# Kernel optimization log

Measured on AMD Instinct MI355X. Metric: run time of the kernel, lower is better.

## Reference

```python
import jax, jax.numpy as jnp
import numpy as np

HEADS, DIM_HEAD = 8, 64
EPS = 1e-5  # torch InstanceNorm1d default


def instance_norm(t):
    # torch InstanceNorm1d(dim_head) applied to (b*h, n, d) normalizes over the
    # last dim d for each (b, h, n); affine=False, biased variance.
    mu = jnp.mean(t, axis=-1, keepdims=True)
    var = jnp.mean((t - mu) ** 2, axis=-1, keepdims=True)
    return (t - mu) * jax.lax.rsqrt(var + EPS)


def setup_inputs() -> dict:
    key = jax.random.key(0)
    k1, k2, k3, k4 = jax.random.split(key, 4)
    B, N, D = 8, 8192, 256
    inner = HEADS * DIM_HEAD  # 512
    x = jax.random.normal(k1, (B, N, D), jnp.float32)
    w_qkv = jax.random.normal(k2, (3 * inner, D), jnp.float32) / np.sqrt(D).astype(np.float32)
    w_out = jax.random.normal(k3, (D, inner), jnp.float32) / np.sqrt(inner).astype(np.float32)
    b_out = 0.01 * jax.random.normal(k4, (D,), jnp.float32)
    return {"x": x, "w_qkv": w_qkv, "w_out": w_out, "b_out": b_out}


def reference(x, w_qkv, w_out, b_out):
    B, N, _ = x.shape
    H, Dh = HEADS, DIM_HEAD
    # fused qkv projection: [B,N,3*H*Dh]
    qkv = jnp.einsum('bnd,ed->bne', x, w_qkv)
    q, k, v = jnp.split(qkv, 3, axis=-1)

    def to_heads(t):
        return t.reshape(B, N, H, Dh).transpose(0, 2, 1, 3)  # b h n d

    q, k, v = to_heads(q), to_heads(k), to_heads(v)
    # galerkin: instance-norm K and V
    k = instance_norm(k)
    v = instance_norm(v)
    # linear (non-softmax) attention: (K^T V) then Q @ (K^T V), scaled by 1/N
    dots = jnp.einsum('bhnd,bhne->bhde', k, v)            # [B,H,Dh,Dh]
    out = jnp.einsum('bhnd,bhde->bhne', q, dots) / N      # [B,H,N,Dh]
    out = out.transpose(0, 2, 1, 3).reshape(B, N, H * Dh)
    return jnp.einsum('bne,de->bnd', out, w_out) + b_out
```

## Files before the change

### kernel.cpp

```cpp
#include <hip/hip_runtime.h>
#include <hip/hip_bf16.h>
#include <stdint.h>

typedef __attribute__((ext_vector_type(8))) __bf16 bf16x8;
typedef __attribute__((ext_vector_type(8))) unsigned short ushort8_t;
typedef __attribute__((ext_vector_type(4))) unsigned short ushort4_t;
typedef __attribute__((ext_vector_type(4))) float f32x4;

#define MFMA16(a, b, c) __builtin_amdgcn_mfma_f32_16x16x32_bf16((a), (b), (c), 0, 0, 0)

static __device__ __forceinline__ unsigned short f2bf(float f) {
  union { float f; unsigned u; } v; v.f = f;
  unsigned r = v.u + 0x7fffu + ((v.u >> 16) & 1u);
  return (unsigned short)(r >> 16);
}
static __device__ __forceinline__ float bf2f(unsigned short u) {
  union { unsigned u; float f; } v; v.u = ((unsigned)u) << 16; return v.f;
}

static __device__ __forceinline__ void gld_lds16(const void* g, void* l) {
  __builtin_amdgcn_global_load_lds((const __attribute__((address_space(1))) void*)g,
                                   (__attribute__((address_space(3))) void*)l, 16, 0, 0);
}

__global__ __launch_bounds__(256) void k_convx(const float* __restrict__ x,
                                               unsigned short* __restrict__ xb) {
  size_t i = ((size_t)blockIdx.x * 256 + threadIdx.x) * 4;
  float4 v = *(const float4*)(x + i);
  ushort4_t o = { f2bf(v.x), f2bf(v.y), f2bf(v.z), f2bf(v.w) };
  *(ushort4_t*)(xb + i) = o;
}

__global__ void k_convw(const float* __restrict__ w, unsigned short* __restrict__ wb) {
  int i = (blockIdx.x * 256 + threadIdx.x) * 4;
  float4 v = *(const float4*)(w + i);
  ushort4_t o = { f2bf(v.x), f2bf(v.y), f2bf(v.z), f2bf(v.w) };
  *(ushort4_t*)(wb + i) = o;
}

__global__ __launch_bounds__(512) void k_gemm1(const unsigned short* __restrict__ xb,
                                               const unsigned short* __restrict__ wqb,
                                               unsigned short* __restrict__ qkv) {
  __shared__ unsigned short As[2][16384];
  __shared__ unsigned short Bs[2][16384];
  const int t = threadIdx.x;
  const int w = t >> 6, lane = t & 63, lr = lane & 15, lg = lane >> 4;
  const int wr = w >> 2, wc = w & 3;

  const int id = blockIdx.x;
  const int nid = (id & 7) * 192 + (id >> 3);
  const int nt = nid % 6, mt = nid / 6;
  const long m0 = (long)mt * 256;
  const int e0 = nt * 256;

  const int srl = lane >> 3, sc = lane & 7;

#pragma unroll
  for (int i = 0; i < 2; ++i) {
    const int r = (w * 2 + i) * 8 + srl;
    const int cs = (sc ^ (r & 7)) << 3;
    gld_lds16(xb + (size_t)(m0 + r) * 256 + cs,          &As[0][(w * 2 + i) * 512]);
    gld_lds16(xb + (size_t)(m0 + 128 + r) * 256 + cs,    &As[0][8192 + (w * 2 + i) * 512]);
    gld_lds16(wqb + (size_t)(e0 + r) * 256 + cs,         &Bs[0][(w * 2 + i) * 512]);
    gld_lds16(wqb + (size_t)(e0 + 128 + r) * 256 + cs,   &Bs[0][8192 + (w * 2 + i) * 512]);
  }
  __syncthreads();

  f32x4 acc[8][4];
#pragma unroll
  for (int i = 0; i < 8; ++i)
#pragma unroll
    for (int j = 0; j < 4; ++j) acc[i][j] = f32x4{0.f, 0.f, 0.f, 0.f};

  bf16x8 a[4][2], b[2][2][2];

  for (int kt = 0; kt < 4; ++kt) {
    const int cur = kt & 1, nxt = cur ^ 1;
    const int kn0 = (kt + 1) * 64;
    const bool st = kt < 3;

#pragma unroll
    for (int mb = 0; mb < 4; ++mb) {
      const int R = wr * 128 + mb * 16 + lr;
#pragma unroll
      for (int kh = 0; kh < 2; ++kh)
        a[mb][kh] = *(const bf16x8*)&As[cur][R * 64 + ((((kh << 2) + lg) ^ (R & 7)) << 3)];
    }
#pragma unroll
    for (int nb = 0; nb < 2; ++nb) {
      const int E = wc * 64 + nb * 16 + lr;
#pragma unroll
      for (int kh = 0; kh < 2; ++kh)
        b[0][nb][kh] = *(const bf16x8*)&Bs[cur][E * 64 + ((((kh << 2) + lg) ^ (E & 7)) << 3)];
    }
    if (st) {
#pragma unroll
      for (int i = 0; i < 2; ++i) {
        const int r = (w * 2 + i) * 8 + srl;
        gld_lds16(xb + (size_t)(m0 + r) * 256 + kn0 + ((sc ^ (r & 7)) << 3),
                  &As[nxt][(w * 2 + i) * 512]);
      }
    }
    __builtin_amdgcn_s_barrier();
    __builtin_amdgcn_s_setprio(1);
#pragma unroll
    for (int mb = 0; mb < 4; ++mb)
#pragma unroll
      for (int nb = 0; nb < 2; ++nb)
#pragma unroll
        for (int kh = 0; kh < 2; ++kh)
          acc[mb][nb] = MFMA16(a[mb][kh], b[0][nb][kh], acc[mb][nb]);
    __builtin_amdgcn_s_setprio(0);
    __builtin_amdgcn_s_barrier();

#pragma unroll
    for (int nb = 0; nb < 2; ++nb) {
      const int E = wc * 64 + 32 + nb * 16 + lr;
#pragma unroll
      for (int kh = 0; kh < 2; ++kh)
        b[1][nb][kh] = *(const bf16x8*)&Bs[cur][E * 64 + ((((kh << 2) + lg) ^ (E & 7)) << 3)];
    }
    if (st) {
#pragma unroll
      for (int i = 0; i < 2; ++i) {
        const int r = (w * 2 + i) * 8 + srl;
        gld_lds16(xb + (size_t)(m0 + 128 + r) * 256 + kn0 + ((sc ^ (r & 7)) << 3),
                  &As[nxt][8192 + (w * 2 + i) * 512]);
      }
    }
    __builtin_amdgcn_s_barrier();
    __builtin_amdgcn_s_setprio(1);
#pragma unroll
    for (int mb = 0; mb < 4; ++mb)
#pragma unroll
      for (int nb = 0; nb < 2; ++nb)
#pragma unroll
        for (int kh = 0; kh < 2; ++kh)
          acc[mb][2 + nb] = MFMA16(a[mb][kh], b[1][nb][kh], acc[mb][2 + nb]);
    __builtin_amdgcn_s_setprio(0);
    __builtin_amdgcn_s_barrier();

#pragma unroll
    for (int mb = 0; mb < 4; ++mb) {
      const int R = wr * 128 + 64 + mb * 16 + lr;
#pragma unroll
      for (int kh = 0; kh < 2; ++kh)
        a[mb][kh] = *(const bf16x8*)&As[cur][R * 64 + ((((kh << 2) + lg) ^ (R & 7)) << 3)];
    }
    if (st) {
#pragma unroll
      for (int i = 0; i < 2; ++i) {
        const int r = (w * 2 + i) * 8 + srl;
        gld_lds16(wqb + (size_t)(e0 + r) * 256 + kn0 + ((sc ^ (r & 7)) << 3),
                  &Bs[nxt][(w * 2 + i) * 512]);
      }
    }
    __builtin_amdgcn_s_barrier();
    __builtin_amdgcn_s_setprio(1);
#pragma unroll
    for (int mb = 0; mb < 4; ++mb)
#pragma unroll
      for (int nb = 0; nb < 2; ++nb)
#pragma unroll
        for (int kh = 0; kh < 2; ++kh)
          acc[4 + mb][nb] = MFMA16(a[mb][kh], b[0][nb][kh], acc[4 + mb][nb]);
    __builtin_amdgcn_s_setprio(0);
    __builtin_amdgcn_s_barrier();

    if (st) {
#pragma unroll
      for (int i = 0; i < 2; ++i) {
        const int r = (w * 2 + i) * 8 + srl;
        gld_lds16(wqb + (size_t)(e0 + 128 + r) * 256 + kn0 + ((sc ^ (r & 7)) << 3),
                  &Bs[nxt][8192 + (w * 2 + i) * 512]);
      }
    }
    __builtin_amdgcn_s_barrier();
    __builtin_amdgcn_s_setprio(1);
#pragma unroll
    for (int mb = 0; mb < 4; ++mb)
#pragma unroll
      for (int nb = 0; nb < 2; ++nb)
#pragma unroll
        for (int kh = 0; kh < 2; ++kh)
          acc[4 + mb][2 + nb] = MFMA16(a[mb][kh], b[1][nb][kh], acc[4 + mb][2 + nb]);
    __builtin_amdgcn_s_setprio(0);
    __syncthreads();
  }

#pragma unroll
  for (int i = 0; i < 8; ++i) {
    const long row0 = m0 + wr * 128 + (i >> 2) * 64 + (i & 3) * 16 + lg * 4;
#pragma unroll
    for (int j = 0; j < 4; ++j) {
      const int col = e0 + wc * 64 + (j >> 1) * 32 + (j & 1) * 16 + lr;
#pragma unroll
      for (int rg = 0; rg < 4; ++rg)
        qkv[(size_t)(row0 + rg) * 1536 + col] = f2bf(acc[i][j][rg]);
    }
  }
}

__global__ __launch_bounds__(256) void k_dots(const unsigned short* __restrict__ qkv,
                                              float* __restrict__ partials) {
  __shared__ unsigned short ktl[2][64 * 72];
  __shared__ unsigned short vtl[2][64 * 72];
  const int bh = blockIdx.x, ch = blockIdx.y;
  const int b = bh >> 3, h = bh & 7;
  const int t = threadIdx.x;
  const int w = t >> 6, lane = t & 63, lr = lane & 15, lg = lane >> 4;
  const unsigned short* kbase = qkv + ((size_t)b * 8192) * 1536 + 512 + h * 64;
  const int r = t >> 2, q4 = t & 3;
  const int n00 = ch * 1024;
  f32x4 acc[4];
#pragma unroll
  for (int eb = 0; eb < 4; ++eb) acc[eb] = f32x4{0.f, 0.f, 0.f, 0.f};

  ushort8_t rA[4], rB[4];
  {
    const unsigned short* krow = kbase + (size_t)(n00 + r) * 1536 + q4 * 16;
    rA[0] = *(const ushort8_t*)krow;
    rA[1] = *(const ushort8_t*)(krow + 8);
    rA[2] = *(const ushort8_t*)(krow + 512);
    rA[3] = *(const ushort8_t*)(krow + 520);
  }

#define DOTS_BODY(RC, RN, NT)                                                     \
  {                                                                               \
    float kf[16], vf[16];                                                         \
    _Pragma("unroll") for (int i = 0; i < 8; ++i) {                               \
      kf[i] = bf2f(RC[0][i]); kf[i + 8] = bf2f(RC[1][i]);                         \
      vf[i] = bf2f(RC[2][i]); vf[i + 8] = bf2f(RC[3][i]);                         \
    }                                                                             \
    float ksum = 0, ksq = 0, vsum = 0, vsq = 0;                                   \
    _Pragma("unroll") for (int i = 0; i < 16; ++i) {                              \
      ksum += kf[i]; ksq += kf[i] * kf[i];                                        \
      vsum += vf[i]; vsq += vf[i] * vf[i];                                        \
    }                                                                             \
    ksum += __shfl_xor(ksum, 1); ksq += __shfl_xor(ksq, 1);                       \
    vsum += __shfl_xor(vsum, 1); vsq += __shfl_xor(vsq, 1);                       \
    ksum += __shfl_xor(ksum, 2); ksq += __shfl_xor(ksq, 2);                       \
    vsum += __shfl_xor(vsum, 2); vsq += __shfl_xor(vsq, 2);                       \
    const float kmean = ksum * (1.f / 64.f);                                      \
    const float krs = rsqrtf(ksq * (1.f / 64.f) - kmean * kmean + 1e-5f);         \
    const float vmean = vsum * (1.f / 64.f);                                      \
    const float vrs = rsqrtf(vsq * (1.f / 64.f) - vmean * vmean + 1e-5f);         \
    const int cu = (NT) & 1;                                                      \
    _Pragma("unroll") for (int i = 0; i < 16; ++i) {                              \
      int d = q4 * 16 + i;                                                        \
      ktl[cu][d * 72 + r] = f2bf((kf[i] - kmean) * krs);                          \
      vtl[cu][d * 72 + r] = f2bf((vf[i] - vmean) * vrs);                          \
    }                                                                             \
    if ((NT) + 1 < 16) {                                                          \
      const unsigned short* krow2 =                                               \
          kbase + (size_t)(n00 + ((NT) + 1) * 64 + r) * 1536 + q4 * 16;           \
      RN[0] = *(const ushort8_t*)krow2;                                           \
      RN[1] = *(const ushort8_t*)(krow2 + 8);                                     \
      RN[2] = *(const ushort8_t*)(krow2 + 512);                                   \
      RN[3] = *(const ushort8_t*)(krow2 + 520);                                   \
    }                                                                             \
    __syncthreads();                                                              \
    _Pragma("unroll") for (int ns = 0; ns < 64; ns += 32) {                       \
      bf16x8 af = *(const bf16x8*)&ktl[cu][(16 * w + lr) * 72 + ns + lg * 8];     \
      _Pragma("unroll") for (int eb = 0; eb < 4; ++eb) {                          \
        bf16x8 bv = *(const bf16x8*)&vtl[cu][(16 * eb + lr) * 72 + ns + lg * 8];  \
        acc[eb] = MFMA16(af, bv, acc[eb]);                                        \
      }                                                                           \
    }                                                                             \
  }

  for (int nt = 0; nt < 16; nt += 2) {
    DOTS_BODY(rA, rB, nt);
    DOTS_BODY(rB, rA, nt + 1);
  }
#undef DOTS_BODY

  float* pb = partials + ((size_t)ch * 64 + bh) * 4096;
#pragma unroll
  for (int eb = 0; eb < 4; ++eb)
#pragma unroll
    for (int rg = 0; rg < 4; ++rg) {
      int d = 16 * w + lg * 4 + rg;
      int e = 16 * eb + lr;
      pb[d * 64 + e] = acc[eb][rg];
    }
}

__global__ __launch_bounds__(256) void k_mmat(const float* __restrict__ partials,
                                              const float* __restrict__ wout,
                                              unsigned short* __restrict__ mswz) {
  __shared__ float dl[4096];
  const int bh = blockIdx.x, b = bh >> 3, h = bh & 7;
  const int t = threadIdx.x;
#pragma unroll
  for (int i = 0; i < 4; ++i) {
    int off = t * 16 + i * 4;
    f32x4 s = {0.f, 0.f, 0.f, 0.f};
    for (int c = 0; c < 8; ++c) {
      f32x4 p = *(const f32x4*)(partials + ((size_t)c * 64 + bh) * 4096 + off);
      s += p;
    }
    *(f32x4*)&dl[off] = s;
  }
  __syncthreads();
  float wrow[64];
#pragma unroll
  for (int e = 0; e < 64; e += 4) {
    f32x4 v = *(const f32x4*)(wout + (size_t)t * 512 + h * 64 + e);
    wrow[e] = v[0]; wrow[e + 1] = v[1]; wrow[e + 2] = v[2]; wrow[e + 3] = v[3];
  }
  const float scale = 1.0f / 8192.0f;
  for (int d = 0; d < 64; ++d) {
    float s = 0.f;
#pragma unroll
    for (int e = 0; e < 64; ++e) s += dl[d * 64 + e] * wrow[e];
    s *= scale;
    int kk = h * 64 + d;
    int kblk = kk >> 5, j = kk & 7;
    int lane8 = ((kk >> 3) & 3) * 16 + (t & 15);
    int nblk = t >> 4;
    mswz[(size_t)b * 131072 + ((size_t)(kblk * 16 + nblk) * 64 + lane8) * 8 + j] = f2bf(s);
  }
}

__global__ __launch_bounds__(512) void k_gemm2(const unsigned short* __restrict__ qkv,
                                               const unsigned short* __restrict__ mswz,
                                               const float* __restrict__ bout,
                                               float* __restrict__ out) {
  __shared__ unsigned short As[2][128 * 64];
  const int b = blockIdx.x >> 6, mt = blockIdx.x & 63;
  const long m0 = (long)mt * 128;
  const int t = threadIdx.x, w = t >> 6, lane = t & 63, lr = lane & 15, lg = lane >> 4;
  const int wr = w >> 2, wc = w & 3;
  const unsigned short* qb = qkv + ((size_t)b * 8192 + m0) * 1536;
  const unsigned short* Mb = mswz + (size_t)b * 131072;
  const int srl = lane >> 3, sc = lane & 7;

#pragma unroll
  for (int i = 0; i < 2; ++i) {
    const int row = (i * 8 + w) * 8 + srl;
    gld_lds16(qb + (size_t)row * 1536 + ((sc ^ (row & 7)) << 3),
              &As[0][(i * 8 + w) * 512]);
  }
  __syncthreads();

  f32x4 acc[4][4];
#pragma unroll
  for (int mb = 0; mb < 4; ++mb)
#pragma unroll
    for (int nb = 0; nb < 4; ++nb) acc[mb][nb] = f32x4{0.f, 0.f, 0.f, 0.f};

  for (int ks = 0; ks < 8; ++ks) {
    const int cur = ks & 1, nxt = cur ^ 1;
    if (ks < 7) {
      const int k0 = (ks + 1) * 64;
#pragma unroll
      for (int i = 0; i < 2; ++i) {
        const int row = (i * 8 + w) * 8 + srl;
        gld_lds16(qb + (size_t)row * 1536 + k0 + ((sc ^ (row & 7)) << 3),
                  &As[nxt][(i * 8 + w) * 512]);
      }
    }
    bf16x8 a[4][2], bfr[2][4];
#pragma unroll
    for (int mb = 0; mb < 4; ++mb) {
      const int R = wr * 64 + mb * 16 + lr;
#pragma unroll
      for (int kh = 0; kh < 2; ++kh)
        a[mb][kh] = *(const bf16x8*)&As[cur][R * 64 + ((((kh << 2) + lg) ^ (R & 7)) << 3)];
    }
#pragma unroll
    for (int kh = 0; kh < 2; ++kh)
#pragma unroll
      for (int nb = 0; nb < 4; ++nb)
        bfr[kh][nb] = *(const bf16x8*)(Mb + ((((size_t)ks * 2 + kh) * 16 + wc * 4 + nb) * 64 + lane) * 8);
#pragma unroll
    for (int mb = 0; mb < 4; ++mb)
#pragma unroll
      for (int nb = 0; nb < 4; ++nb)
#pragma unroll
        for (int kh = 0; kh < 2; ++kh)
          acc[mb][nb] = MFMA16(a[mb][kh], bfr[kh][nb], acc[mb][nb]);
    __syncthreads();
  }

  float bo[4];
#pragma unroll
  for (int nb = 0; nb < 4; ++nb) bo[nb] = bout[wc * 64 + nb * 16 + lr];
  float* ob = out + ((size_t)b * 8192 + m0) * 256;
#pragma unroll
  for (int mb = 0; mb < 4; ++mb)
#pragma unroll
    for (int nb = 0; nb < 4; ++nb)
#pragma unroll
      for (int rg = 0; rg < 4; ++rg) {
        int row = wr * 64 + mb * 16 + lg * 4 + rg;
        int c = wc * 64 + nb * 16 + lr;
        ob[(size_t)row * 256 + c] = acc[mb][nb][rg] + bo[nb];
      }
}

extern "C" void kernel_launch(void* const* d_in, const int* in_sizes, int n_in,
                              void* d_out, int out_size, void* d_ws, size_t ws_size,
                              hipStream_t stream) {
  const float* x    = (const float*)d_in[0];
  const float* wqkv = (const float*)d_in[1];
  const float* wout = (const float*)d_in[2];
  const float* bout = (const float*)d_in[3];
  float* out = (float*)d_out;

  char* ws = (char*)d_ws;
  unsigned short* qkvb = (unsigned short*)ws;
  size_t off = (size_t)65536 * 1536 * 2;
  unsigned short* wqb = (unsigned short*)(ws + off);
  off += (size_t)1536 * 256 * 2;
  float* partials = (float*)(ws + off);
  off += (size_t)8 * 64 * 4096 * 4;
  unsigned short* mswz = (unsigned short*)(ws + off);
  off += (size_t)8 * 131072 * 2;
  unsigned short* xb = (unsigned short*)(ws + off);
  off += (size_t)65536 * 256 * 2;

  k_convx<<<16384, 256, 0, stream>>>(x, xb);
  k_convw<<<384, 256, 0, stream>>>(wqkv, wqb);
  k_gemm1<<<1536, 512, 0, stream>>>(xb, wqb, qkvb);
  dim3 gd(64, 8);
  k_dots<<<gd, 256, 0, stream>>>(qkvb, partials);
  k_mmat<<<64, 256, 0, stream>>>(partials, wout, mswz);
  k_gemm2<<<512, 512, 0, stream>>>(qkvb, mswz, bout, out);
}
```

Before: 195.2 us.

## Fold Q projection into per-batch output matrix, skip computing Q

Instead of materialising Q through the first GEMM, the Q weight slice is folded algebraically into a per-batch 256x256 matrix P = W_out * (dots^T W_q / N) built by the new k_mmat/k_pmat kernels. The first GEMM now only produces K and V (1024 columns), and the final GEMM reads bf16 x with K=256 instead of Q with K=512. This removes a third of the large projection GEMM and its write, and halves the output GEMM's reduction and reads. In exchange it adds two small kernels, an extra bf16 rounding of the fused matrix, and a W_out conversion.

```diff
diff --git a/kernel.cpp b/kernel.cpp
--- a/kernel.cpp
+++ b/kernel.cpp
@@ -38,9 +38,16 @@
   *(ushort4_t*)(wb + i) = o;
 }
 
+__global__ void k_convo(const float* __restrict__ w, unsigned short* __restrict__ wb) {
+  int i = (blockIdx.x * 256 + threadIdx.x) * 4;
+  float4 v = *(const float4*)(w + i);
+  ushort4_t o = { f2bf(v.x), f2bf(v.y), f2bf(v.z), f2bf(v.w) };
+  *(ushort4_t*)(wb + i) = o;
+}
+
 __global__ __launch_bounds__(512) void k_gemm1(const unsigned short* __restrict__ xb,
                                                const unsigned short* __restrict__ wqb,
-                                               unsigned short* __restrict__ qkv) {
+                                               unsigned short* __restrict__ kvb) {
   __shared__ unsigned short As[2][16384];
   __shared__ unsigned short Bs[2][16384];
   const int t = threadIdx.x;
@@ -48,10 +55,10 @@
   const int wr = w >> 2, wc = w & 3;
 
   const int id = blockIdx.x;
-  const int nid = (id & 7) * 192 + (id >> 3);
-  const int nt = nid % 6, mt = nid / 6;
+  const int nid = (id & 7) * 128 + (id >> 3);
+  const int nt = nid & 3, mt = nid >> 2;
   const long m0 = (long)mt * 256;
-  const int e0 = nt * 256;
+  const int e0 = 512 + nt * 256;
 
   const int srl = lane >> 3, sc = lane & 7;
 
@@ -193,15 +200,15 @@
     const long row0 = m0 + wr * 128 + (i >> 2) * 64 + (i & 3) * 16 + lg * 4;
 #pragma unroll
     for (int j = 0; j < 4; ++j) {
-      const int col = e0 + wc * 64 + (j >> 1) * 32 + (j & 1) * 16 + lr;
+      const int col = nt * 256 + wc * 64 + (j >> 1) * 32 + (j & 1) * 16 + lr;
 #pragma unroll
       for (int rg = 0; rg < 4; ++rg)
-        qkv[(size_t)(row0 + rg) * 1536 + col] = f2bf(acc[i][j][rg]);
-    }
-  }
-}
-
-__global__ __launch_bounds__(256) void k_dots(const unsigned short* __restrict__ qkv,
+        kvb[(size_t)(row0 + rg) * 1024 + col] = f2bf(acc[i][j][rg]);
+    }
+  }
+}
+
+__global__ __launch_bounds__(256) void k_dots(const unsigned short* __restrict__ kvb,
                                               float* __restrict__ partials) {
   __shared__ unsigned short ktl[2][64 * 72];
   __shared__ unsigned short vtl[2][64 * 72];
@@ -209,7 +216,7 @@
   const int b = bh >> 3, h = bh & 7;
   const int t = threadIdx.x;
   const int w = t >> 6, lane = t & 63, lr = lane & 15, lg = lane >> 4;
-  const unsigned short* kbase = qkv + ((size_t)b * 8192) * 1536 + 512 + h * 64;
+  const unsigned short* kbase = kvb + ((size_t)b * 8192) * 1024 + h * 64;
   const int r = t >> 2, q4 = t & 3;
   const int n00 = ch * 1024;
   f32x4 acc[4];
@@ -218,7 +225,7 @@
 
   ushort8_t rA[4], rB[4];
   {
-    const unsigned short* krow = kbase + (size_t)(n00 + r) * 1536 + q4 * 16;
+    const unsigned short* krow = kbase + (size_t)(n00 + r) * 1024 + q4 * 16;
     rA[0] = *(const ushort8_t*)krow;
     rA[1] = *(const ushort8_t*)(krow + 8);
     rA[2] = *(const ushort8_t*)(krow + 512);
@@ -253,7 +260,7 @@
     }                                                                             \
     if ((NT) + 1 < 16) {                                                          \
       const unsigned short* krow2 =                                               \
-          kbase + (size_t)(n00 + ((NT) + 1) * 64 + r) * 1536 + q4 * 16;           \
+          kbase + (size_t)(n00 + ((NT) + 1) * 64 + r) * 1024 + q4 * 16;           \
       RN[0] = *(const ushort8_t*)krow2;                                           \
       RN[1] = *(const ushort8_t*)(krow2 + 8);                                     \
       RN[2] = *(const ushort8_t*)(krow2 + 512);                                   \
@@ -287,9 +294,10 @@
 }
 
 __global__ __launch_bounds__(256) void k_mmat(const float* __restrict__ partials,
-                                              const float* __restrict__ wout,
-                                              unsigned short* __restrict__ mswz) {
+                                              const float* __restrict__ wqkv,
+                                              unsigned short* __restrict__ tmpT) {
   __shared__ float dl[4096];
+  __shared__ float wqls[64 * 256];
   const int bh = blockIdx.x, b = bh >> 3, h = bh & 7;
   const int t = threadIdx.x;
 #pragma unroll
@@ -302,29 +310,79 @@
     }
     *(f32x4*)&dl[off] = s;
   }
+#pragma unroll
+  for (int i = 0; i < 16; ++i) {
+    int idx4 = i * 256 + t;
+    int d = idx4 >> 6, c4 = idx4 & 63;
+    *(f32x4*)&wqls[d * 256 + c4 * 4] =
+        *(const f32x4*)(wqkv + (size_t)(h * 64 + d) * 256 + c4 * 4);
+  }
   __syncthreads();
-  float wrow[64];
-#pragma unroll
-  for (int e = 0; e < 64; e += 4) {
-    f32x4 v = *(const f32x4*)(wout + (size_t)t * 512 + h * 64 + e);
-    wrow[e] = v[0]; wrow[e + 1] = v[1]; wrow[e + 2] = v[2]; wrow[e + 3] = v[3];
-  }
+  const int k = t;
   const float scale = 1.0f / 8192.0f;
-  for (int d = 0; d < 64; ++d) {
+  float res[64];
+  for (int e = 0; e < 64; ++e) {
     float s = 0.f;
 #pragma unroll
-    for (int e = 0; e < 64; ++e) s += dl[d * 64 + e] * wrow[e];
-    s *= scale;
-    int kk = h * 64 + d;
-    int kblk = kk >> 5, j = kk & 7;
-    int lane8 = ((kk >> 3) & 3) * 16 + (t & 15);
-    int nblk = t >> 4;
-    mswz[(size_t)b * 131072 + ((size_t)(kblk * 16 + nblk) * 64 + lane8) * 8 + j] = f2bf(s);
-  }
-}
-
-__global__ __launch_bounds__(512) void k_gemm2(const unsigned short* __restrict__ qkv,
-                                               const unsigned short* __restrict__ mswz,
+    for (int d = 0; d < 64; ++d) s += dl[d * 64 + e] * wqls[d * 256 + k];
+    res[e] = s * scale;
+  }
+  unsigned short* dst = tmpT + (size_t)b * 131072 + (size_t)k * 512 + h * 64;
+#pragma unroll
+  for (int e8 = 0; e8 < 8; ++e8) {
+    ushort8_t o;
+#pragma unroll
+    for (int j = 0; j < 8; ++j) o[j] = f2bf(res[e8 * 8 + j]);
+    *(ushort8_t*)(dst + e8 * 8) = o;
+  }
+}
+
+__global__ __launch_bounds__(256) void k_pmat(const unsigned short* __restrict__ woutb,
+                                              const unsigned short* __restrict__ tmpT,
+                                              unsigned short* __restrict__ pswz) {
+  const int bid = blockIdx.x;
+  const int b = bid >> 2, oq = (bid >> 1) & 1, kq = bid & 1;
+  const int t = threadIdx.x, w = t >> 6, lane = t & 63, lr = lane & 15, lg = lane >> 4;
+  const int wr = w >> 1, wc = w & 1;
+  const int ob = oq * 128 + wr * 64, kb = kq * 128 + wc * 64;
+  const unsigned short* tb = tmpT + (size_t)b * 131072;
+
+  f32x4 acc[4][4];
+#pragma unroll
+  for (int mb = 0; mb < 4; ++mb)
+#pragma unroll
+    for (int nb = 0; nb < 4; ++nb) acc[mb][nb] = f32x4{0.f, 0.f, 0.f, 0.f};
+
+  for (int ks = 0; ks < 16; ++ks) {
+    bf16x8 a[4], bb[4];
+#pragma unroll
+    for (int mb = 0; mb < 4; ++mb)
+      a[mb] = *(const bf16x8*)(woutb + (size_t)(ob + mb * 16 + lr) * 512 + ks * 32 + lg * 8);
+#pragma unroll
+    for (int nb = 0; nb < 4; ++nb)
+      bb[nb] = *(const bf16x8*)(tb + (size_t)(kb + nb * 16 + lr) * 512 + ks * 32 + lg * 8);
+#pragma unroll
+    for (int mb = 0; mb < 4; ++mb)
+#pragma unroll
+      for (int nb = 0; nb < 4; ++nb) acc[mb][nb] = MFMA16(a[mb], bb[nb], acc[mb][nb]);
+  }
+
+  unsigned short* pb = pswz + (size_t)b * 65536;
+#pragma unroll
+  for (int mb = 0; mb < 4; ++mb)
+#pragma unroll
+    for (int nb = 0; nb < 4; ++nb)
+#pragma unroll
+      for (int rg = 0; rg < 4; ++rg) {
+        int o = ob + mb * 16 + lg * 4 + rg;
+        int k = kb + nb * 16 + lr;
+        pb[(((k >> 5) * 16 + (o >> 4)) * 64 + (o & 15) + ((k >> 3) & 3) * 16) * 8 + (k & 7)] =
+            f2bf(acc[mb][nb][rg]);
+      }
+}
+
+__global__ __launch_bounds__(512) void k_gemm2(const unsigned short* __restrict__ xb,
+                                               const unsigned short* __restrict__ pswz,
                                                const float* __restrict__ bout,
                                                float* __restrict__ out) {
   __shared__ unsigned short As[2][128 * 64];
@@ -332,14 +390,14 @@
   const long m0 = (long)mt * 128;
   const int t = threadIdx.x, w = t >> 6, lane = t & 63, lr = lane & 15, lg = lane >> 4;
   const int wr = w >> 2, wc = w & 3;
-  const unsigned short* qb = qkv + ((size_t)b * 8192 + m0) * 1536;
-  const unsigned short* Mb = mswz + (size_t)b * 131072;
+  const unsigned short* qb = xb + ((size_t)b * 8192 + m0) * 256;
+  const unsigned short* Mb = pswz + (size_t)b * 65536;
   const int srl = lane >> 3, sc = lane & 7;
 
 #pragma unroll
   for (int i = 0; i < 2; ++i) {
     const int row = (i * 8 + w) * 8 + srl;
-    gld_lds16(qb + (size_t)row * 1536 + ((sc ^ (row & 7)) << 3),
+    gld_lds16(qb + (size_t)row * 256 + ((sc ^ (row & 7)) << 3),
               &As[0][(i * 8 + w) * 512]);
   }
   __syncthreads();
@@ -350,14 +408,14 @@
 #pragma unroll
     for (int nb = 0; nb < 4; ++nb) acc[mb][nb] = f32x4{0.f, 0.f, 0.f, 0.f};
 
-  for (int ks = 0; ks < 8; ++ks) {
+  for (int ks = 0; ks < 4; ++ks) {
     const int cur = ks & 1, nxt = cur ^ 1;
-    if (ks < 7) {
+    if (ks < 3) {
       const int k0 = (ks + 1) * 64;
 #pragma unroll
       for (int i = 0; i < 2; ++i) {
         const int row = (i * 8 + w) * 8 + srl;
-        gld_lds16(qb + (size_t)row * 1536 + k0 + ((sc ^ (row & 7)) << 3),
+        gld_lds16(qb + (size_t)row * 256 + k0 + ((sc ^ (row & 7)) << 3),
                   &As[nxt][(i * 8 + w) * 512]);
       }
     }
@@ -410,22 +468,28 @@
   float* out = (float*)d_out;
 
   char* ws = (char*)d_ws;
-  unsigned short* qkvb = (unsigned short*)ws;
-  size_t off = (size_t)65536 * 1536 * 2;
+  unsigned short* kvb = (unsigned short*)ws;
+  size_t off = (size_t)65536 * 1024 * 2;
+  unsigned short* xb = (unsigned short*)(ws + off);
+  off += (size_t)65536 * 256 * 2;
   unsigned short* wqb = (unsigned short*)(ws + off);
   off += (size_t)1536 * 256 * 2;
+  unsigned short* woutb = (unsigned short*)(ws + off);
+  off += (size_t)256 * 512 * 2;
   float* partials = (float*)(ws + off);
   off += (size_t)8 * 64 * 4096 * 4;
-  unsigned short* mswz = (unsigned short*)(ws + off);
+  unsigned short* tmpT = (unsigned short*)(ws + off);
   off += (size_t)8 * 131072 * 2;
-  unsigned short* xb = (unsigned short*)(ws + off);
-  off += (size_t)65536 * 256 * 2;
+  unsigned short* pswz = (unsigned short*)(ws + off);
+  off += (size_t)8 * 65536 * 2;
 
   k_convx<<<16384, 256, 0, stream>>>(x, xb);
   k_convw<<<384, 256, 0, stream>>>(wqkv, wqb);
-  k_gemm1<<<1536, 512, 0, stream>>>(xb, wqb, qkvb);
+  k_convo<<<128, 256, 0, stream>>>(wout, woutb);
+  k_gemm1<<<1024, 512, 0, stream>>>(xb, wqb, kvb);
   dim3 gd(64, 8);
-  k_dots<<<gd, 256, 0, stream>>>(qkvb, partials);
-  k_mmat<<<64, 256, 0, stream>>>(partials, wout, mswz);
-  k_gemm2<<<512, 512, 0, stream>>>(qkvb, mswz, bout, out);
-}
+  k_dots<<<gd, 256, 0, stream>>>(kvb, partials);
+  k_mmat<<<64, 256, 0, stream>>>(partials, wqkv, tmpT);
+  k_pmat<<<32, 256, 0, stream>>>(woutb, tmpT, pswz);
+  k_gemm2<<<512, 512, 0, stream>>>(xb, pswz, bout, out);
+}
```

After: 183.9 us. 1.06x faster.
